# Kernel optimization log

Measured on AMD Instinct MI355X. Metric: run time of the kernel, lower is better.

The kernel has to match this reference:

```python
import jax, jax.numpy as jnp
import numpy as np


def setup_inputs() -> dict:
    key = jax.random.key(0)
    kx, kw = jax.random.split(key)
    x = jax.random.normal(kx, (4, 2048, 4096), dtype=jnp.float32)
    weight = jax.random.normal(kw, (4096, 4096), dtype=jnp.float32) * 0.02
    return {"x": x, "weight": weight}


def _binact(x):
    """BiReal piecewise sign approximation with STE: forward = sign(x),
    backward flows through the clipped quadratic surrogate out3."""
    m1 = x < -1.0
    m2 = x < 0.0
    m3 = x < 1.0
    out1 = jnp.where(m1, -1.0, x * x + 2.0 * x)
    out2 = jnp.where(m2, out1, -x * x + 2.0 * x)
    out3 = jnp.where(m3, out2, 1.0)
    return jax.lax.stop_gradient(jnp.sign(x) - out3) + out3


def _quant_weight(w):
    """Per-output-row mean-abs scale * sign(w), STE through clamp(w,-1,1)."""
    scale = jax.lax.stop_gradient(jnp.mean(jnp.abs(w), axis=1, keepdims=True))
    bw_no_grad = scale * jnp.sign(w)  # [out, in]
    clipped = jnp.clip(w, -1.0, 1.0)
    return jax.lax.stop_gradient(bw_no_grad - clipped) + clipped


def reference(x, weight):
    xq = _binact(x)               # [B, S, in]
    wq = _quant_weight(weight)    # [out, in]
    # F.linear(input, w) with no bias: x @ w.T
    return jnp.einsum('bsi,oi->bso', xq, wq)
```

## Files before the change

kernel.cpp:

```cpp
#include <hip/hip_runtime.h>
#include <stdint.h>

typedef __attribute__((ext_vector_type(4))) int i32x4;
typedef __attribute__((ext_vector_type(8))) int i32x8;
typedef __attribute__((ext_vector_type(16))) float f32x16;

#define BM 128
#define BN 128

__device__ __forceinline__ uint32_t nib4(float v) {
  return v > 0.f ? 0x2u : (v < 0.f ? 0xAu : 0u);
}

__device__ __forceinline__ uint32_t pack8(float4 a, float4 b) {
  return nib4(a.x) | (nib4(a.y) << 4) | (nib4(a.z) << 8) | (nib4(a.w) << 12) |
         (nib4(b.x) << 16) | (nib4(b.y) << 20) | (nib4(b.z) << 24) | (nib4(b.w) << 28);
}

__global__ __launch_bounds__(256) void quant_fused_kernel(
    const float4* __restrict__ x, uint32_t* __restrict__ xq,
    const float4* __restrict__ w, uint32_t* __restrict__ wq,
    float* __restrict__ scale, int N, int K) {
  const int t = threadIdx.x;
  const int b = blockIdx.x;

  if (b < N) {
    const float4* wr = w + (size_t)b * (K / 4);
    uint32_t* wo = wq + (size_t)b * (K / 8);
    float asum = 0.f;
    for (int p = t; p < K / 8; p += 256) {
      float4 a = wr[2 * p];
      float4 c = wr[2 * p + 1];
      wo[p] = pack8(a, c);
      asum += fabsf(a.x) + fabsf(a.y) + fabsf(a.z) + fabsf(a.w) +
              fabsf(c.x) + fabsf(c.y) + fabsf(c.z) + fabsf(c.w);
    }
    for (int off = 32; off > 0; off >>= 1) asum += __shfl_down(asum, off);
    __shared__ float red[4];
    if ((t & 63) == 0) red[t >> 6] = asum;
    __syncthreads();
    if (t == 0) scale[b] = (red[0] + red[1] + red[2] + red[3]) / (float)K;
  } else {
    const size_t base = (size_t)(b - N) * 1024;
#pragma unroll
    for (int j = 0; j < 4; ++j) {
      size_t p = base + (size_t)j * 256 + t;
      float4 a = x[2 * p];
      float4 c = x[2 * p + 1];
      xq[p] = pack8(a, c);
    }
  }
}

__device__ __forceinline__ void load16(const uint8_t* g, uint8_t* l) {
  __builtin_amdgcn_global_load_lds(
      (const __attribute__((address_space(1))) uint32_t*)(uintptr_t)g,
      (__attribute__((address_space(3))) uint32_t*)(uintptr_t)l,
      16, 0, 0);
}

__global__ __launch_bounds__(256, 3) void gemm_bt_kernel(
    const uint8_t* __restrict__ A, const uint8_t* __restrict__ B,
    const float* __restrict__ scale, float* __restrict__ C,
    int M, int N, int K) {
  __shared__ __align__(16) uint8_t As[BM * 64];
  __shared__ __align__(16) uint8_t Bs[BN * 64];

  const int tid = threadIdx.x;
  const int lane = tid & 63;
  const int wave = tid >> 6;
  const int waveM = wave & 1;
  const int waveN = wave >> 1;

  const int rowA0 = blockIdx.y * BM;
  const int rowB0 = blockIdx.x * BN;

  const int KB = K / 2;

  const uint8_t* aG = A + (size_t)(rowA0 + wave * 32 + (lane >> 2)) * KB + (lane & 3) * 16;
  const uint8_t* bG = B + (size_t)(rowB0 + wave * 32 + (lane >> 2)) * KB + (lane & 3) * 16;
  uint8_t* aL = As + wave * 2048 + lane * 16;
  uint8_t* bL = Bs + wave * 2048 + lane * 16;
  const size_t strideG16 = (size_t)16 * KB;

  const uint8_t* aF = As + (size_t)(waveM * 64 + (lane & 31)) * 64 + (lane >> 5) * 16;
  const uint8_t* bF = Bs + (size_t)(waveN * 64 + (lane & 31)) * 64 + (lane >> 5) * 16;

  f32x16 acc[2][2] = {};
  i32x8 aop[2] = {}, bop[2] = {};

  for (int kb = 0; kb < KB; kb += 64) {
    __syncthreads();
    load16(aG + kb, aL);
    load16(aG + kb + strideG16, aL + 1024);
    load16(bG + kb, bL);
    load16(bG + kb + strideG16, bL + 1024);
    __syncthreads();

#pragma unroll
    for (int s = 0; s < 2; ++s) {
#pragma unroll
      for (int mi = 0; mi < 2; ++mi) {
        i32x4 t = *(const i32x4*)(aF + mi * 32 * 64 + s * 32);
        aop[mi].s0 = t.x; aop[mi].s1 = t.y; aop[mi].s2 = t.z; aop[mi].s3 = t.w;
      }
#pragma unroll
      for (int ni = 0; ni < 2; ++ni) {
        i32x4 t = *(const i32x4*)(bF + ni * 32 * 64 + s * 32);
        bop[ni].s0 = t.x; bop[ni].s1 = t.y; bop[ni].s2 = t.z; bop[ni].s3 = t.w;
      }
#pragma unroll
      for (int mi = 0; mi < 2; ++mi)
#pragma unroll
        for (int ni = 0; ni < 2; ++ni)
          acc[mi][ni] = __builtin_amdgcn_mfma_scale_f32_32x32x64_f8f6f4(
              aop[mi], bop[ni], acc[mi][ni],
               4,  4,
               0, 0x7f7f7f7f,  0, 0x7f7f7f7f);
    }
  }

  const int cCol = rowB0 + waveN * 64 + (lane & 31);
  const int cRowBase = rowA0 + waveM * 64 + 4 * (lane >> 5);
  float sc[2];
#pragma unroll
  for (int ni = 0; ni < 2; ++ni) sc[ni] = scale[cCol + ni * 32];
#pragma unroll
  for (int mi = 0; mi < 2; ++mi)
#pragma unroll
    for (int ni = 0; ni < 2; ++ni)
#pragma unroll
      for (int r = 0; r < 16; ++r) {
        int row = cRowBase + mi * 32 + (r & 3) + 8 * (r >> 2);
        C[(size_t)row * N + cCol + ni * 32] = acc[mi][ni][r] * sc[ni];
      }
}

__global__ void fallback_gemm(const float* __restrict__ X, const float* __restrict__ W,
                              float* __restrict__ C, int M, int N, int K) {
  __shared__ float xs[16][65];
  __shared__ float ws[16][65];
  __shared__ float wabs[256];
  __shared__ float scl[16];
  const int tx = threadIdx.x, ty = threadIdx.y;
  const int t = ty * 16 + tx;
  float acc = 0.f, wa = 0.f;
  for (int k0 = 0; k0 < K; k0 += 64) {
    __syncthreads();
#pragma unroll
    for (int j = 0; j < 4; ++j) {
      int e = t * 4 + j;
      int r = e >> 6, c = e & 63;
      float xv = X[(size_t)(blockIdx.y * 16 + r) * K + k0 + c];
      xs[r][c] = xv > 0.f ? 1.f : (xv < 0.f ? -1.f : 0.f);
      float wv = W[(size_t)(blockIdx.x * 16 + r) * K + k0 + c];
      ws[r][c] = wv > 0.f ? 1.f : (wv < 0.f ? -1.f : 0.f);
      wa += fabsf(wv);
    }
    __syncthreads();
#pragma unroll 8
    for (int k = 0; k < 64; ++k) acc += xs[ty][k] * ws[tx][k];
  }
  wabs[t] = wa;
  __syncthreads();
  for (int s2 = 8; s2 > 0; s2 >>= 1) {
    if (tx < s2) wabs[t] += wabs[t + s2];
    __syncthreads();
  }
  if (tx == 0) scl[ty] = wabs[t] / (float)K;
  __syncthreads();
  C[(size_t)(blockIdx.y * 16 + ty) * N + (blockIdx.x * 16 + tx)] = acc * scl[tx];
}

extern "C" void kernel_launch(void* const* d_in, const int* in_sizes, int n_in,
                              void* d_out, int out_size, void* d_ws, size_t ws_size,
                              hipStream_t stream) {
  const float* x = (const float*)d_in[0];
  const float* w = (const float*)d_in[1];
  float* out = (float*)d_out;

  const int K = 4096;
  const int N = in_sizes[1] / K;
  const int M = in_sizes[0] / K;

  size_t need = (size_t)M * (K / 2) + (size_t)N * (K / 2) + (size_t)N * sizeof(float);
  if (ws_size >= need) {
    uint8_t* Xq = (uint8_t*)d_ws;
    uint8_t* Wq = Xq + (size_t)M * (K / 2);
    float* scale = (float*)(Wq + (size_t)N * (K / 2));

    const int xBlocks = (int)(((size_t)M * K) / 8192);
    quant_fused_kernel<<<N + xBlocks, 256, 0, stream>>>(
        (const float4*)x, (uint32_t*)Xq, (const float4*)w, (uint32_t*)Wq, scale, N, K);

    dim3 grid(N / BN, M / BM);
    gemm_bt_kernel<<<grid, 256, 0, stream>>>(Xq, Wq, scale, out, M, N, K);
  } else {
    dim3 grid(N / 16, M / 16);
    fallback_gemm<<<grid, dim3(16, 16), 0, stream>>>(x, w, out, M, N, K);
  }
}
```

Before: 344.8 us.

## Pre-tile quantized operands into MFMA fragment layout and swizzle GEMM block order

The quantization kernel now writes the packed FP4 X and W into a blocked layout of 32-row by 128-k tiles, so each GEMM wave loads a contiguous 2 KB chunk per k-step. LDS fragment reads also become contiguous per lane. The GEMM additionally remaps workgroup IDs in groups of eight to improve L2 reuse. Quant threads now handle 32 elements each with 128-bit stores, though the transposed access pattern for X reads may be less coalesced.

```diff
diff --git a/kernel.cpp b/kernel.cpp
--- a/kernel.cpp
+++ b/kernel.cpp
@@ -17,37 +17,54 @@
          (nib4(b.x) << 16) | (nib4(b.y) << 20) | (nib4(b.z) << 24) | (nib4(b.w) << 28);
 }
 
+__device__ __forceinline__ float abs4(float4 v) {
+  return fabsf(v.x) + fabsf(v.y) + fabsf(v.z) + fabsf(v.w);
+}
+
 __global__ __launch_bounds__(256) void quant_fused_kernel(
-    const float4* __restrict__ x, uint32_t* __restrict__ xq,
-    const float4* __restrict__ w, uint32_t* __restrict__ wq,
-    float* __restrict__ scale, int N, int K) {
+    const float4* __restrict__ x, uint4* __restrict__ xq,
+    const float4* __restrict__ w, uint4* __restrict__ wq,
+    float* __restrict__ scale, int halfN, int K, int kbShift) {
   const int t = threadIdx.x;
   const int b = blockIdx.x;
-
-  if (b < N) {
-    const float4* wr = w + (size_t)b * (K / 4);
-    uint32_t* wo = wq + (size_t)b * (K / 8);
-    float asum = 0.f;
-    for (int p = t; p < K / 8; p += 256) {
-      float4 a = wr[2 * p];
-      float4 c = wr[2 * p + 1];
-      wo[p] = pack8(a, c);
-      asum += fabsf(a.x) + fabsf(a.y) + fabsf(a.z) + fabsf(a.w) +
-              fabsf(c.x) + fabsf(c.y) + fabsf(c.z) + fabsf(c.w);
-    }
+  const int kbT = K >> 7;
+
+  if (b < halfN) {
+    const int row = b * 2 + (t >> 7);
+    const int tt = t & 127;
+    const float4* src = w + ((size_t)row * K >> 2) + tt * 8;
+    float4 v0 = src[0], v1 = src[1], v2 = src[2], v3 = src[3];
+    float4 v4 = src[4], v5 = src[5], v6 = src[6], v7 = src[7];
+    uint4 o;
+    o.x = pack8(v0, v1); o.y = pack8(v2, v3);
+    o.z = pack8(v4, v5); o.w = pack8(v6, v7);
+    size_t fi = ((size_t)(row >> 5) * kbT + (tt >> 2)) * 128 + (tt & 3) * 32 + (row & 31);
+    wq[fi] = o;
+    float asum = abs4(v0) + abs4(v1) + abs4(v2) + abs4(v3) +
+                 abs4(v4) + abs4(v5) + abs4(v6) + abs4(v7);
     for (int off = 32; off > 0; off >>= 1) asum += __shfl_down(asum, off);
     __shared__ float red[4];
     if ((t & 63) == 0) red[t >> 6] = asum;
     __syncthreads();
-    if (t == 0) scale[b] = (red[0] + red[1] + red[2] + red[3]) / (float)K;
+    if ((t & 127) == 0) scale[row] = (red[t >> 6] + red[(t >> 6) + 1]) / (float)K;
   } else {
-    const size_t base = (size_t)(b - N) * 1024;
+    const size_t base = (size_t)(b - halfN) * 1024;
 #pragma unroll
     for (int j = 0; j < 4; ++j) {
-      size_t p = base + (size_t)j * 256 + t;
-      float4 a = x[2 * p];
-      float4 c = x[2 * p + 1];
-      xq[p] = pack8(a, c);
+      size_t f = base + (size_t)j * 256 + t;
+      size_t g = f >> 7;
+      int p2 = (int)(f & 127);
+      size_t rowblk = g >> kbShift;
+      int kbblk = (int)(g & (kbT - 1));
+      size_t row = rowblk * 32 + (p2 & 31);
+      int k32 = kbblk * 4 + (p2 >> 5);
+      const float4* src = x + ((size_t)row * K >> 2) + k32 * 8;
+      float4 v0 = src[0], v1 = src[1], v2 = src[2], v3 = src[3];
+      float4 v4 = src[4], v5 = src[5], v6 = src[6], v7 = src[7];
+      uint4 o;
+      o.x = pack8(v0, v1); o.y = pack8(v2, v3);
+      o.z = pack8(v4, v5); o.w = pack8(v6, v7);
+      xq[f] = o;
     }
   }
 }
@@ -71,43 +88,45 @@
   const int wave = tid >> 6;
   const int waveM = wave & 1;
   const int waveN = wave >> 1;
-
-  const int rowA0 = blockIdx.y * BM;
-  const int rowB0 = blockIdx.x * BN;
-
-  const int KB = K / 2;
-
-  const uint8_t* aG = A + (size_t)(rowA0 + wave * 32 + (lane >> 2)) * KB + (lane & 3) * 16;
-  const uint8_t* bG = B + (size_t)(rowB0 + wave * 32 + (lane >> 2)) * KB + (lane & 3) * 16;
+  const int kbT = K >> 7;
+
+  const int nwg = gridDim.x * gridDim.y;
+  const int id = blockIdx.y * gridDim.x + blockIdx.x;
+  const int swz = (id & 7) * (nwg >> 3) + (id >> 3);
+  const int bx = swz % gridDim.x;
+  const int by = swz / gridDim.x;
+
+  const uint8_t* aG = A + ((size_t)(by * 4 + wave) * kbT) * 2048 + lane * 16;
+  const uint8_t* bG = B + ((size_t)(bx * 4 + wave) * kbT) * 2048 + lane * 16;
   uint8_t* aL = As + wave * 2048 + lane * 16;
   uint8_t* bL = Bs + wave * 2048 + lane * 16;
-  const size_t strideG16 = (size_t)16 * KB;
-
-  const uint8_t* aF = As + (size_t)(waveM * 64 + (lane & 31)) * 64 + (lane >> 5) * 16;
-  const uint8_t* bF = Bs + (size_t)(waveN * 64 + (lane & 31)) * 64 + (lane >> 5) * 16;
+
+  const uint8_t* aF = As + waveM * 4096 + lane * 16;
+  const uint8_t* bF = Bs + waveN * 4096 + lane * 16;
 
   f32x16 acc[2][2] = {};
   i32x8 aop[2] = {}, bop[2] = {};
 
-  for (int kb = 0; kb < KB; kb += 64) {
-    __syncthreads();
-    load16(aG + kb, aL);
-    load16(aG + kb + strideG16, aL + 1024);
-    load16(bG + kb, bL);
-    load16(bG + kb + strideG16, bL + 1024);
+  for (int i = 0; i < kbT; ++i) {
+    __syncthreads();
+    const size_t o = (size_t)i * 2048;
+    load16(aG + o, aL);
+    load16(aG + o + 1024, aL + 1024);
+    load16(bG + o, bL);
+    load16(bG + o + 1024, bL + 1024);
     __syncthreads();
 
 #pragma unroll
     for (int s = 0; s < 2; ++s) {
 #pragma unroll
       for (int mi = 0; mi < 2; ++mi) {
-        i32x4 t = *(const i32x4*)(aF + mi * 32 * 64 + s * 32);
-        aop[mi].s0 = t.x; aop[mi].s1 = t.y; aop[mi].s2 = t.z; aop[mi].s3 = t.w;
+        i32x4 t4 = *(const i32x4*)(aF + mi * 2048 + s * 1024);
+        aop[mi].s0 = t4.x; aop[mi].s1 = t4.y; aop[mi].s2 = t4.z; aop[mi].s3 = t4.w;
       }
 #pragma unroll
       for (int ni = 0; ni < 2; ++ni) {
-        i32x4 t = *(const i32x4*)(bF + ni * 32 * 64 + s * 32);
-        bop[ni].s0 = t.x; bop[ni].s1 = t.y; bop[ni].s2 = t.z; bop[ni].s3 = t.w;
+        i32x4 t4 = *(const i32x4*)(bF + ni * 2048 + s * 1024);
+        bop[ni].s0 = t4.x; bop[ni].s1 = t4.y; bop[ni].s2 = t4.z; bop[ni].s3 = t4.w;
       }
 #pragma unroll
       for (int mi = 0; mi < 2; ++mi)
@@ -120,8 +139,8 @@
     }
   }
 
-  const int cCol = rowB0 + waveN * 64 + (lane & 31);
-  const int cRowBase = rowA0 + waveM * 64 + 4 * (lane >> 5);
+  const int cCol = bx * BN + waveN * 64 + (lane & 31);
+  const int cRowBase = by * BM + waveM * 64 + 4 * (lane >> 5);
   float sc[2];
 #pragma unroll
   for (int ni = 0; ni < 2; ++ni) sc[ni] = scale[cCol + ni * 32];
@@ -189,9 +208,13 @@
     uint8_t* Wq = Xq + (size_t)M * (K / 2);
     float* scale = (float*)(Wq + (size_t)N * (K / 2));
 
-    const int xBlocks = (int)(((size_t)M * K) / 8192);
-    quant_fused_kernel<<<N + xBlocks, 256, 0, stream>>>(
-        (const float4*)x, (uint32_t*)Xq, (const float4*)w, (uint32_t*)Wq, scale, N, K);
+    const int kbT = K >> 7;
+    const int kbShift = __builtin_ctz(kbT);
+    const int halfN = N / 2;
+    const int xBlocks = (int)(((size_t)M * K / 32) / 1024);
+    quant_fused_kernel<<<halfN + xBlocks, 256, 0, stream>>>(
+        (const float4*)x, (uint4*)Xq, (const float4*)w, (uint4*)Wq,
+        scale, halfN, K, kbShift);
 
     dim3 grid(N / BN, M / BM);
     gemm_bt_kernel<<<grid, 256, 0, stream>>>(Xq, Wq, scale, out, M, N, K);
```

Measured after the change: 344.9 us. About the same (+0.0%).
